# Performance work log

Measured on AMD Instinct MI355X. Metric: run time of the kernel, lower is better.

Reference implementation:

```python
import jax, jax.numpy as jnp
import numpy as np

B_SZ, L, N, H = 8, 4096, 256, 256
R_MIN, R_MAX, MAX_PHASE = 0.0, 1.0, 0.314


def setup_inputs() -> dict:
    key = jax.random.key(0)
    ks = jax.random.split(key, 8)
    x = jax.random.normal(ks[0], (B_SZ, L, H), jnp.float32)
    def glorot(k, shape):
        return jax.random.normal(k, shape, jnp.float32) * jnp.sqrt(2.0 / (shape[0] + shape[1])).astype(jnp.float32)
    B_re = glorot(ks[1], (N, H))
    B_im = glorot(ks[2], (N, H))
    C_re = glorot(ks[3], (H, N))
    C_im = glorot(ks[4], (H, N))
    # DiskRingRadius / DiskRingPhase initializers
    u1 = jax.random.uniform(ks[5], (N,), jnp.float32, 1e-6, 1.0)
    u2 = jax.random.uniform(ks[6], (N,), jnp.float32, 1e-6, 1.0)
    nu_log = jnp.log(-0.5 * jnp.log(u1 * (R_MAX ** 2 - R_MIN ** 2) + R_MIN ** 2))
    theta_log = jnp.log(MAX_PHASE * u2)
    D = jax.random.normal(ks[7], (H,), jnp.float32) * 0.05  # RandomNormal(stddev=0.05)
    return dict(x=x, B_re=B_re, B_im=B_im, C_re=C_re, C_im=C_im,
                nu_log=nu_log, theta_log=theta_log, D=D)


def reference(x, B_re, B_im, C_re, C_im, nu_log, theta_log, D):
    # Diagonal complex recurrence parameters
    Lambda = jnp.exp(jax.lax.complex(-jnp.exp(nu_log), jnp.exp(theta_log)))  # [N]
    gamma = jnp.sqrt(1.0 - jnp.abs(Lambda) ** 2).astype(jnp.complex64)       # [N]
    B_norm = (B_re + 1j * B_im).astype(jnp.complex64) * gamma[:, None]       # [N,H]
    C = (C_re + 1j * C_im).astype(jnp.complex64)                             # [H,N]

    # Input projection: [B,L,N] complex
    Bu = jnp.einsum('blh,nh->bln', x.astype(jnp.complex64), B_norm)
    Lambda_el = jnp.broadcast_to(Lambda, Bu.shape)

    def combine(a, b):
        la, ba = a
        lb, bb = b
        return (la * lb, lb * ba + bb)

    _, states = jax.lax.associative_scan(combine, (Lambda_el, Bu), axis=1)  # [B,L,N]

    y = jnp.real(jnp.einsum('bln,hn->blh', states, C))
    y = y + x * D  # H_in == H -> elementwise skip
    return y
```

## Files before the change

### kernel.cpp

```cpp
#include <hip/hip_runtime.h>
#include <hip/hip_bf16.h>
#include <math.h>

#define B_SZ 8
#define LSEQ 4096
#define NDIM 256
#define HDIM 256
#define MROWS (B_SZ * LSEQ)
#define CH 64
#define NC (LSEQ / CH)

#define BM 64
#define BN 128
#define BK 32
#define PAD 40
#define SSTR 68

typedef _Float16 half8 __attribute__((ext_vector_type(8)));
typedef _Float16 half4 __attribute__((ext_vector_type(4)));
typedef float fx4 __attribute__((ext_vector_type(4)));

__global__ void k_prep(const float* __restrict__ Bre, const float* __restrict__ Bim,
                       const float* __restrict__ Cre, const float* __restrict__ Cim,
                       const float* __restrict__ nu_log, const float* __restrict__ th_log,
                       _Float16* __restrict__ BreH, _Float16* __restrict__ BimH,
                       _Float16* __restrict__ CreH, _Float16* __restrict__ CimNH,
                       float* __restrict__ lamRe, float* __restrict__ lamIm,
                       float* __restrict__ powRe, float* __restrict__ powIm,
                       float* __restrict__ powCRe, float* __restrict__ powCIm) {
    int r = blockIdx.x;
    int t = threadIdx.x;
    float nu  = expf(nu_log[r]);
    float th  = expf(th_log[r]);
    float mod = expf(-nu);
    float g   = sqrtf(fmaxf(1.0f - mod * mod, 0.0f));
    if (t == 0) {
        lamRe[r] = mod * cosf(th);
        lamIm[r] = mod * sinf(th);
    }
    int i = r * 256 + t;
    BreH[i]  = (_Float16)(Bre[i] * g);
    BimH[i]  = (_Float16)(Bim[i] * g);
    CreH[i]  = (_Float16)Cre[i];
    CimNH[i] = (_Float16)(-Cim[i]);
    float nuN = expf(nu_log[t]);
    float thN = expf(th_log[t]);
    if (r < CH) {
        float k  = (float)(r + 1);
        float mo = expf(-nuN * k);
        powRe[r * 256 + t] = mo * cosf(thN * k);
        powIm[r * 256 + t] = mo * sinf(thN * k);
        float kc = (float)(CH * r);
        float mc = expf(-nuN * kc);
        powCRe[r * 256 + t] = mc * cosf(thN * kc);
        powCIm[r * 256 + t] = mc * sinf(thN * kc);
    }
}

__launch_bounds__(256)
__global__ void k_buscan(const float* __restrict__ x,
                         const _Float16* __restrict__ BreH,
                         const _Float16* __restrict__ BimH,
                         const float* __restrict__ lamRe,
                         const float* __restrict__ lamIm,
                         _Float16* __restrict__ stReH,
                         _Float16* __restrict__ stImH,
                         float* __restrict__ finRe,
                         float* __restrict__ finIm) {
    __shared__ __align__(16) _Float16 smem[25600];

    const int tid  = threadIdx.x;
    const int lane = tid & 63;
    const int wave = tid >> 6;
    const int wr   = wave >> 1;
    const int wc   = wave & 1;
    const int m0   = blockIdx.x * BM;
    const int n0   = blockIdx.y * BN;

    const int ar = tid >> 2, ac = (tid & 3) * 8;
    const int br = tid >> 1, bc = (tid & 1) * 16;

    const int fRC = lane & 15;
    const int fKg = (lane >> 4) * 8;

    fx4 accR[8], accI[8];
#pragma unroll
    for (int i = 0; i < 8; ++i) { accR[i] = (fx4)0.0f; accI[i] = (fx4)0.0f; }

    float4 xf0, xf1;
    half8 w0, w1, w2, w3;

    {
        const float* xp = x + (size_t)(m0 + ar) * HDIM + ac;
        xf0 = *(const float4*)xp;
        xf1 = *(const float4*)(xp + 4);
        const _Float16* bp1 = BreH + (size_t)(n0 + br) * HDIM + bc;
        const _Float16* bp2 = BimH + (size_t)(n0 + br) * HDIM + bc;
        w0 = *(const half8*)bp1;  w1 = *(const half8*)(bp1 + 8);
        w2 = *(const half8*)bp2;  w3 = *(const half8*)(bp2 + 8);
        half8 hv;
        hv[0]=(_Float16)xf0.x; hv[1]=(_Float16)xf0.y; hv[2]=(_Float16)xf0.z; hv[3]=(_Float16)xf0.w;
        hv[4]=(_Float16)xf1.x; hv[5]=(_Float16)xf1.y; hv[6]=(_Float16)xf1.z; hv[7]=(_Float16)xf1.w;
        *(half8*)&smem[ar * PAD + ac] = hv;
        *(half8*)&smem[2560 + br * PAD + bc] = w0;  *(half8*)&smem[2560 + br * PAD + bc + 8] = w1;
        *(half8*)&smem[7680 + br * PAD + bc] = w2;  *(half8*)&smem[7680 + br * PAD + bc + 8] = w3;
    }
    __syncthreads();

    int p = 0;
    for (int k0 = 0; k0 < HDIM; k0 += BK) {
        const int po = p * 12800;
        const bool nx = (k0 + BK) < HDIM;
        if (nx) {
            const float* xp = x + (size_t)(m0 + ar) * HDIM + k0 + BK + ac;
            xf0 = *(const float4*)xp;
            xf1 = *(const float4*)(xp + 4);
            const _Float16* bp1 = BreH + (size_t)(n0 + br) * HDIM + k0 + BK + bc;
            const _Float16* bp2 = BimH + (size_t)(n0 + br) * HDIM + k0 + BK + bc;
            w0 = *(const half8*)bp1;  w1 = *(const half8*)(bp1 + 8);
            w2 = *(const half8*)bp2;  w3 = *(const half8*)(bp2 + 8);
        }
        half8 af[2], bRf[4], bIf[4];
#pragma unroll
        for (int sm = 0; sm < 2; ++sm)
            af[sm] = *(const half8*)&smem[po + (wr * 32 + sm * 16 + fRC) * PAD + fKg];
#pragma unroll
        for (int sn = 0; sn < 4; ++sn) {
            bRf[sn] = *(const half8*)&smem[po + 2560 + (wc * 64 + sn * 16 + fRC) * PAD + fKg];
            bIf[sn] = *(const half8*)&smem[po + 7680 + (wc * 64 + sn * 16 + fRC) * PAD + fKg];
        }
#pragma unroll
        for (int sm = 0; sm < 2; ++sm)
#pragma unroll
            for (int sn = 0; sn < 4; ++sn) {
                accR[sm * 4 + sn] = __builtin_amdgcn_mfma_f32_16x16x32_f16(af[sm], bRf[sn], accR[sm * 4 + sn], 0, 0, 0);
                accI[sm * 4 + sn] = __builtin_amdgcn_mfma_f32_16x16x32_f16(af[sm], bIf[sn], accI[sm * 4 + sn], 0, 0, 0);
            }
        if (nx) {
            const int qo = (p ^ 1) * 12800;
            half8 hv;
            hv[0]=(_Float16)xf0.x; hv[1]=(_Float16)xf0.y; hv[2]=(_Float16)xf0.z; hv[3]=(_Float16)xf0.w;
            hv[4]=(_Float16)xf1.x; hv[5]=(_Float16)xf1.y; hv[6]=(_Float16)xf1.z; hv[7]=(_Float16)xf1.w;
            *(half8*)&smem[qo + ar * PAD + ac] = hv;
            *(half8*)&smem[qo + 2560 + br * PAD + bc] = w0;  *(half8*)&smem[qo + 2560 + br * PAD + bc + 8] = w1;
            *(half8*)&smem[qo + 7680 + br * PAD + bc] = w2;  *(half8*)&smem[qo + 7680 + br * PAD + bc + 8] = w3;
        }
        __syncthreads();
        p ^= 1;
    }

    _Float16* SRe = smem;
    _Float16* SIm = smem + 8704;

    const int rBase = (lane >> 4) * 4;
#pragma unroll
    for (int sm = 0; sm < 2; ++sm)
#pragma unroll
        for (int sn = 0; sn < 4; ++sn) {
            int col = wc * 64 + sn * 16 + fRC;
            int row = wr * 32 + sm * 16 + rBase;
            half4 h1, h2;
#pragma unroll
            for (int reg = 0; reg < 4; ++reg) {
                h1[reg] = (_Float16)accR[sm * 4 + sn][reg];
                h2[reg] = (_Float16)accI[sm * 4 + sn][reg];
            }
            *(half4*)&SRe[col * SSTR + row] = h1;
            *(half4*)&SIm[col * SSTR + row] = h2;
        }
    __syncthreads();

    if (tid < BN) {
        int col = tid;
        int n = n0 + col;
        float lr = lamRe[n], li = lamIm[n];
        _Float16* cR = &SRe[col * SSTR];
        _Float16* cI = &SIm[col * SSTR];
        float sr = 0.0f, si = 0.0f;
#pragma unroll 8
        for (int r = 0; r < CH; ++r) {
            float ur = (float)cR[r];
            float ui = (float)cI[r];
            float nr = fmaf(lr, sr, fmaf(-li, si, ur));
            float ni = fmaf(lr, si, fmaf(li, sr, ui));
            sr = nr; si = ni;
            cR[r] = (_Float16)sr;
            cI[r] = (_Float16)si;
        }
        int bb = blockIdx.x >> 6, cc = blockIdx.x & 63;
        size_t f = ((size_t)(bb * NC + cc)) * NDIM + n;
        finRe[f] = sr;
        finIm[f] = si;
    }
    __syncthreads();

    {
        int row = tid >> 2;
        int cb  = (tid & 3) * 32;
        size_t gbase = (size_t)(m0 + row) * NDIM + n0 + cb;
#pragma unroll
        for (int g = 0; g < 4; ++g) {
            half8 h1, h2;
#pragma unroll
            for (int e = 0; e < 8; ++e) {
                int col = cb + g * 8 + e;
                h1[e] = SRe[col * SSTR + row];
                h2[e] = SIm[col * SSTR + row];
            }
            *(half8*)(stReH + gbase + g * 8) = h1;
            *(half8*)(stImH + gbase + g * 8) = h2;
        }
    }
}

__launch_bounds__(256)
__global__ void k_out(const _Float16* __restrict__ sReH,
                      const _Float16* __restrict__ sImH,
                      const _Float16* __restrict__ CreH,
                      const _Float16* __restrict__ CimNH,
                      const float* __restrict__ powRe,
                      const float* __restrict__ powIm,
                      const float* __restrict__ powCRe,
                      const float* __restrict__ powCIm,
                      const float* __restrict__ finRe,
                      const float* __restrict__ finIm,
                      const float* __restrict__ x,
                      const float* __restrict__ Dv,
                      float* __restrict__ y) {
    __shared__ __align__(16) _Float16 A1[2][BM * PAD];
    __shared__ __align__(16) _Float16 A2[2][BM * PAD];
    __shared__ __align__(16) _Float16 Cr[2][BN * PAD];
    __shared__ __align__(16) _Float16 Ci[2][BN * PAD];
    __shared__ __align__(16) float carL[2][NDIM];

    const int tid  = threadIdx.x;
    const int lane = tid & 63;
    const int wave = tid >> 6;
    const int wr   = wave >> 1;
    const int wc   = wave & 1;
    const int m0   = blockIdx.x * BM;
    const int h0   = blockIdx.y * BN;
    const int bb   = blockIdx.x >> 6;
    const int cc   = blockIdx.x & 63;

    const int ar = tid >> 2, ac = (tid & 3) * 8;
    const int br = tid >> 1, bc = (tid & 1) * 16;

    const int fRC = lane & 15;
    const int fKg = (lane >> 4) * 8;

    {
        const int n = tid;
        float cr = 0.0f, ci = 0.0f;
#pragma unroll 4
        for (int j = 0; j < cc; ++j) {
            int k = cc - 1 - j;
            float pr = powCRe[k * NDIM + n];
            float pi = powCIm[k * NDIM + n];
            size_t f = ((size_t)(bb * NC + j)) * NDIM + n;
            float fr = finRe[f];
            float fi = finIm[f];
            cr = fmaf(pr, fr, fmaf(-pi, fi, cr));
            ci = fmaf(pr, fi, fmaf( pi, fr, ci));
        }
        carL[0][n] = cr;
        carL[1][n] = ci;
    }
    __syncthreads();

    fx4 acc[8];
#pragma unroll
    for (int i = 0; i < 8; ++i) acc[i] = (fx4)0.0f;

    half8 s1, s2, c0a, c0b, c1a, c1b;
    float4 pr0, pr1, pi0, pi1, cr0, cr1, ci0, ci1;

#define LOAD_STAGE(K0)                                                          \
    {                                                                           \
        size_t aOff = (size_t)(m0 + ar) * NDIM + (K0) + ac;                     \
        s1 = *(const half8*)(sReH + aOff);                                      \
        s2 = *(const half8*)(sImH + aOff);                                      \
        size_t pOff = (size_t)ar * NDIM + (K0) + ac;                            \
        pr0 = *(const float4*)(powRe + pOff); pr1 = *(const float4*)(powRe + pOff + 4); \
        pi0 = *(const float4*)(powIm + pOff); pi1 = *(const float4*)(powIm + pOff + 4); \
        cr0 = *(const float4*)&carL[0][(K0) + ac]; cr1 = *(const float4*)&carL[0][(K0) + ac + 4]; \
        ci0 = *(const float4*)&carL[1][(K0) + ac]; ci1 = *(const float4*)&carL[1][(K0) + ac + 4]; \
        const _Float16* cp1 = CreH  + (size_t)(h0 + br) * NDIM + (K0) + bc;     \
        const _Float16* cp2 = CimNH + (size_t)(h0 + br) * NDIM + (K0) + bc;     \
        c0a = *(const half8*)cp1;  c0b = *(const half8*)(cp1 + 8);              \
        c1a = *(const half8*)cp2;  c1b = *(const half8*)(cp2 + 8);              \
    }

#define WRITE_STAGE(P)                                                          \
    {                                                                           \
        float prA[8] = {pr0.x,pr0.y,pr0.z,pr0.w,pr1.x,pr1.y,pr1.z,pr1.w};       \
        float piA[8] = {pi0.x,pi0.y,pi0.z,pi0.w,pi1.x,pi1.y,pi1.z,pi1.w};       \
        float crA[8] = {cr0.x,cr0.y,cr0.z,cr0.w,cr1.x,cr1.y,cr1.z,cr1.w};       \
        float ciA[8] = {ci0.x,ci0.y,ci0.z,ci0.w,ci1.x,ci1.y,ci1.z,ci1.w};       \
        half8 h1, h2;                                                           \
        _Pragma("unroll")                                                       \
        for (int e = 0; e < 8; ++e) {                                           \
            float ur = fmaf(prA[e], crA[e], fmaf(-piA[e], ciA[e], (float)s1[e])); \
            float ui = fmaf(prA[e], ciA[e], fmaf( piA[e], crA[e], (float)s2[e])); \
            h1[e] = (_Float16)ur; h2[e] = (_Float16)ui;                         \
        }                                                                       \
        *(half8*)&A1[P][ar * PAD + ac] = h1;                                    \
        *(half8*)&A2[P][ar * PAD + ac] = h2;                                    \
        *(half8*)&Cr[P][br * PAD + bc] = c0a;  *(half8*)&Cr[P][br * PAD + bc + 8] = c0b; \
        *(half8*)&Ci[P][br * PAD + bc] = c1a;  *(half8*)&Ci[P][br * PAD + bc + 8] = c1b; \
    }

    LOAD_STAGE(0);
    WRITE_STAGE(0);
    __syncthreads();

    int p = 0;
    for (int k0 = 0; k0 < NDIM; k0 += BK) {
        const bool nx = (k0 + BK) < NDIM;
        if (nx) LOAD_STAGE(k0 + BK);
        half8 a1[2], a2[2], bRf[4], bIf[4];
#pragma unroll
        for (int sm = 0; sm < 2; ++sm) {
            a1[sm] = *(const half8*)&A1[p][(wr * 32 + sm * 16 + fRC) * PAD + fKg];
            a2[sm] = *(const half8*)&A2[p][(wr * 32 + sm * 16 + fRC) * PAD + fKg];
        }
#pragma unroll
        for (int sn = 0; sn < 4; ++sn) {
            bRf[sn] = *(const half8*)&Cr[p][(wc * 64 + sn * 16 + fRC) * PAD + fKg];
            bIf[sn] = *(const half8*)&Ci[p][(wc * 64 + sn * 16 + fRC) * PAD + fKg];
        }
#pragma unroll
        for (int sm = 0; sm < 2; ++sm)
#pragma unroll
            for (int sn = 0; sn < 4; ++sn) {
                acc[sm * 4 + sn] = __builtin_amdgcn_mfma_f32_16x16x32_f16(a1[sm], bRf[sn], acc[sm * 4 + sn], 0, 0, 0);
                acc[sm * 4 + sn] = __builtin_amdgcn_mfma_f32_16x16x32_f16(a2[sm], bIf[sn], acc[sm * 4 + sn], 0, 0, 0);
            }
        if (nx) WRITE_STAGE(p ^ 1);
        __syncthreads();
        p ^= 1;
    }

    float d[4];
#pragma unroll
    for (int sn = 0; sn < 4; ++sn) d[sn] = Dv[h0 + wc * 64 + sn * 16 + fRC];

    const int rBase = (lane >> 4) * 4;
#pragma unroll
    for (int sm = 0; sm < 2; ++sm)
#pragma unroll
        for (int sn = 0; sn < 4; ++sn) {
            int h = h0 + wc * 64 + sn * 16 + fRC;
#pragma unroll
            for (int reg = 0; reg < 4; ++reg) {
                int m = m0 + wr * 32 + sm * 16 + rBase + reg;
                size_t idx = (size_t)m * HDIM + h;
                y[idx] = fmaf(x[idx], d[sn], acc[sm * 4 + sn][reg]);
            }
        }
#undef LOAD_STAGE
#undef WRITE_STAGE
}

extern "C" void kernel_launch(void* const* d_in, const int* in_sizes, int n_in,
                              void* d_out, int out_size, void* d_ws, size_t ws_size,
                              hipStream_t stream) {
    const float* x      = (const float*)d_in[0];
    const float* B_re   = (const float*)d_in[1];
    const float* B_im   = (const float*)d_in[2];
    const float* C_re   = (const float*)d_in[3];
    const float* C_im   = (const float*)d_in[4];
    const float* nu_log = (const float*)d_in[5];
    const float* th_log = (const float*)d_in[6];
    const float* D      = (const float*)d_in[7];
    float* y = (float*)d_out;

    char* p = (char*)d_ws;
    _Float16* stReH = (_Float16*)p;  p += (size_t)MROWS * NDIM * 2;
    _Float16* stImH = (_Float16*)p;  p += (size_t)MROWS * NDIM * 2;
    _Float16* BreH  = (_Float16*)p;  p += (size_t)NDIM * HDIM * 2;
    _Float16* BimH  = (_Float16*)p;  p += (size_t)NDIM * HDIM * 2;
    _Float16* CreH  = (_Float16*)p;  p += (size_t)HDIM * NDIM * 2;
    _Float16* CimNH = (_Float16*)p;  p += (size_t)HDIM * NDIM * 2;
    float* lamRe  = (float*)p;  p += NDIM * 4;
    float* lamIm  = (float*)p;  p += NDIM * 4;
    float* powRe  = (float*)p;  p += (size_t)CH * NDIM * 4;
    float* powIm  = (float*)p;  p += (size_t)CH * NDIM * 4;
    float* powCRe = (float*)p;  p += (size_t)NC * NDIM * 4;
    float* powCIm = (float*)p;  p += (size_t)NC * NDIM * 4;
    float* finRe  = (float*)p;  p += (size_t)B_SZ * NC * NDIM * 4;
    float* finIm  = (float*)p;  p += (size_t)B_SZ * NC * NDIM * 4;

    k_prep<<<NDIM, 256, 0, stream>>>(B_re, B_im, C_re, C_im, nu_log, th_log,
                                     BreH, BimH, CreH, CimNH, lamRe, lamIm,
                                     powRe, powIm, powCRe, powCIm);

    dim3 gGemm(MROWS / BM, NDIM / BN);
    k_buscan<<<gGemm, 256, 0, stream>>>(x, BreH, BimH, lamRe, lamIm,
                                        stReH, stImH, finRe, finIm);

    dim3 gOut(MROWS / BM, HDIM / BN);
    k_out<<<gOut, 256, 0, stream>>>(stReH, stImH, CreH, CimNH,
                                    powRe, powIm, powCRe, powCIm,
                                    finRe, finIm, x, D, y);
}
```

Before: 164.0 us.

## Load A fragments directly from global and single-buffer weights to cut LDS

In both GEMM kernels the activation (A) operand is now read straight from global memory into MFMA fragment registers instead of going through shared memory. The weight tiles move from double-buffered to single-buffered LDS, with two barriers per k-step. LDS use drops and launch bounds request 4 blocks per CU, aiming at higher occupancy and fewer LDS round trips. The cost is less coalesced global loads for A, more barriers, and no overlap from double buffering.

```diff
diff --git a/kernel.cpp b/kernel.cpp
--- a/kernel.cpp
+++ b/kernel.cpp
@@ -57,7 +57,7 @@
     }
 }
 
-__launch_bounds__(256)
+__launch_bounds__(256, 4)
 __global__ void k_buscan(const float* __restrict__ x,
                          const _Float16* __restrict__ BreH,
                          const _Float16* __restrict__ BimH,
@@ -67,7 +67,7 @@
                          _Float16* __restrict__ stImH,
                          float* __restrict__ finRe,
                          float* __restrict__ finIm) {
-    __shared__ __align__(16) _Float16 smem[25600];
+    __shared__ __align__(16) _Float16 smem[17408];
 
     const int tid  = threadIdx.x;
     const int lane = tid & 63;
@@ -77,57 +77,53 @@
     const int m0   = blockIdx.x * BM;
     const int n0   = blockIdx.y * BN;
 
-    const int ar = tid >> 2, ac = (tid & 3) * 8;
     const int br = tid >> 1, bc = (tid & 1) * 16;
 
     const int fRC = lane & 15;
     const int fKg = (lane >> 4) * 8;
+    const int rowL0 = wr * 32 + fRC;
 
     fx4 accR[8], accI[8];
 #pragma unroll
     for (int i = 0; i < 8; ++i) { accR[i] = (fx4)0.0f; accI[i] = (fx4)0.0f; }
 
-    float4 xf0, xf1;
     half8 w0, w1, w2, w3;
-
     {
-        const float* xp = x + (size_t)(m0 + ar) * HDIM + ac;
-        xf0 = *(const float4*)xp;
-        xf1 = *(const float4*)(xp + 4);
         const _Float16* bp1 = BreH + (size_t)(n0 + br) * HDIM + bc;
         const _Float16* bp2 = BimH + (size_t)(n0 + br) * HDIM + bc;
         w0 = *(const half8*)bp1;  w1 = *(const half8*)(bp1 + 8);
         w2 = *(const half8*)bp2;  w3 = *(const half8*)(bp2 + 8);
-        half8 hv;
-        hv[0]=(_Float16)xf0.x; hv[1]=(_Float16)xf0.y; hv[2]=(_Float16)xf0.z; hv[3]=(_Float16)xf0.w;
-        hv[4]=(_Float16)xf1.x; hv[5]=(_Float16)xf1.y; hv[6]=(_Float16)xf1.z; hv[7]=(_Float16)xf1.w;
-        *(half8*)&smem[ar * PAD + ac] = hv;
-        *(half8*)&smem[2560 + br * PAD + bc] = w0;  *(half8*)&smem[2560 + br * PAD + bc + 8] = w1;
-        *(half8*)&smem[7680 + br * PAD + bc] = w2;  *(half8*)&smem[7680 + br * PAD + bc + 8] = w3;
-    }
-    __syncthreads();
-
-    int p = 0;
+    }
+
     for (int k0 = 0; k0 < HDIM; k0 += BK) {
-        const int po = p * 12800;
+        *(half8*)&smem[br * PAD + bc] = w0;
+        *(half8*)&smem[br * PAD + bc + 8] = w1;
+        *(half8*)&smem[5120 + br * PAD + bc] = w2;
+        *(half8*)&smem[5120 + br * PAD + bc + 8] = w3;
         const bool nx = (k0 + BK) < HDIM;
         if (nx) {
-            const float* xp = x + (size_t)(m0 + ar) * HDIM + k0 + BK + ac;
-            xf0 = *(const float4*)xp;
-            xf1 = *(const float4*)(xp + 4);
             const _Float16* bp1 = BreH + (size_t)(n0 + br) * HDIM + k0 + BK + bc;
             const _Float16* bp2 = BimH + (size_t)(n0 + br) * HDIM + k0 + BK + bc;
             w0 = *(const half8*)bp1;  w1 = *(const half8*)(bp1 + 8);
             w2 = *(const half8*)bp2;  w3 = *(const half8*)(bp2 + 8);
         }
-        half8 af[2], bRf[4], bIf[4];
-#pragma unroll
-        for (int sm = 0; sm < 2; ++sm)
-            af[sm] = *(const half8*)&smem[po + (wr * 32 + sm * 16 + fRC) * PAD + fKg];
+        half8 af[2];
+#pragma unroll
+        for (int sm = 0; sm < 2; ++sm) {
+            const float* xp = x + (size_t)(m0 + rowL0 + sm * 16) * HDIM + k0 + fKg;
+            float4 f0 = *(const float4*)xp;
+            float4 f1 = *(const float4*)(xp + 4);
+            half8 hv;
+            hv[0]=(_Float16)f0.x; hv[1]=(_Float16)f0.y; hv[2]=(_Float16)f0.z; hv[3]=(_Float16)f0.w;
+            hv[4]=(_Float16)f1.x; hv[5]=(_Float16)f1.y; hv[6]=(_Float16)f1.z; hv[7]=(_Float16)f1.w;
+            af[sm] = hv;
+        }
+        __syncthreads();
+        half8 bRf[4], bIf[4];
 #pragma unroll
         for (int sn = 0; sn < 4; ++sn) {
-            bRf[sn] = *(const half8*)&smem[po + 2560 + (wc * 64 + sn * 16 + fRC) * PAD + fKg];
-            bIf[sn] = *(const half8*)&smem[po + 7680 + (wc * 64 + sn * 16 + fRC) * PAD + fKg];
+            bRf[sn] = *(const half8*)&smem[(wc * 64 + sn * 16 + fRC) * PAD + fKg];
+            bIf[sn] = *(const half8*)&smem[5120 + (wc * 64 + sn * 16 + fRC) * PAD + fKg];
         }
 #pragma unroll
         for (int sm = 0; sm < 2; ++sm)
@@ -136,17 +132,7 @@
                 accR[sm * 4 + sn] = __builtin_amdgcn_mfma_f32_16x16x32_f16(af[sm], bRf[sn], accR[sm * 4 + sn], 0, 0, 0);
                 accI[sm * 4 + sn] = __builtin_amdgcn_mfma_f32_16x16x32_f16(af[sm], bIf[sn], accI[sm * 4 + sn], 0, 0, 0);
             }
-        if (nx) {
-            const int qo = (p ^ 1) * 12800;
-            half8 hv;
-            hv[0]=(_Float16)xf0.x; hv[1]=(_Float16)xf0.y; hv[2]=(_Float16)xf0.z; hv[3]=(_Float16)xf0.w;
-            hv[4]=(_Float16)xf1.x; hv[5]=(_Float16)xf1.y; hv[6]=(_Float16)xf1.z; hv[7]=(_Float16)xf1.w;
-            *(half8*)&smem[qo + ar * PAD + ac] = hv;
-            *(half8*)&smem[qo + 2560 + br * PAD + bc] = w0;  *(half8*)&smem[qo + 2560 + br * PAD + bc + 8] = w1;
-            *(half8*)&smem[qo + 7680 + br * PAD + bc] = w2;  *(half8*)&smem[qo + 7680 + br * PAD + bc + 8] = w3;
-        }
         __syncthreads();
-        p ^= 1;
     }
 
     _Float16* SRe = smem;
@@ -213,7 +199,7 @@
     }
 }
 
-__launch_bounds__(256)
+__launch_bounds__(256, 4)
 __global__ void k_out(const _Float16* __restrict__ sReH,
                       const _Float16* __restrict__ sImH,
                       const _Float16* __restrict__ CreH,
@@ -227,10 +213,8 @@
                       const float* __restrict__ x,
                       const float* __restrict__ Dv,
                       float* __restrict__ y) {
-    __shared__ __align__(16) _Float16 A1[2][BM * PAD];
-    __shared__ __align__(16) _Float16 A2[2][BM * PAD];
-    __shared__ __align__(16) _Float16 Cr[2][BN * PAD];
-    __shared__ __align__(16) _Float16 Ci[2][BN * PAD];
+    __shared__ __align__(16) _Float16 Cr[BN * PAD];
+    __shared__ __align__(16) _Float16 Ci[BN * PAD];
     __shared__ __align__(16) float carL[2][NDIM];
 
     const int tid  = threadIdx.x;
@@ -243,11 +227,18 @@
     const int bb   = blockIdx.x >> 6;
     const int cc   = blockIdx.x & 63;
 
-    const int ar = tid >> 2, ac = (tid & 3) * 8;
     const int br = tid >> 1, bc = (tid & 1) * 16;
-
     const int fRC = lane & 15;
     const int fKg = (lane >> 4) * 8;
+    const int rowL0 = wr * 32 + fRC;
+
+    half8 w0, w1, w2, w3;
+    {
+        const _Float16* cp1 = CreH  + (size_t)(h0 + br) * NDIM + bc;
+        const _Float16* cp2 = CimNH + (size_t)(h0 + br) * NDIM + bc;
+        w0 = *(const half8*)cp1;  w1 = *(const half8*)(cp1 + 8);
+        w2 = *(const half8*)cp2;  w3 = *(const half8*)(cp2 + 8);
+    }
 
     {
         const int n = tid;
@@ -272,62 +263,53 @@
 #pragma unroll
     for (int i = 0; i < 8; ++i) acc[i] = (fx4)0.0f;
 
-    half8 s1, s2, c0a, c0b, c1a, c1b;
-    float4 pr0, pr1, pi0, pi1, cr0, cr1, ci0, ci1;
-
-#define LOAD_STAGE(K0)                                                          \
-    {                                                                           \
-        size_t aOff = (size_t)(m0 + ar) * NDIM + (K0) + ac;                     \
-        s1 = *(const half8*)(sReH + aOff);                                      \
-        s2 = *(const half8*)(sImH + aOff);                                      \
-        size_t pOff = (size_t)ar * NDIM + (K0) + ac;                            \
-        pr0 = *(const float4*)(powRe + pOff); pr1 = *(const float4*)(powRe + pOff + 4); \
-        pi0 = *(const float4*)(powIm + pOff); pi1 = *(const float4*)(powIm + pOff + 4); \
-        cr0 = *(const float4*)&carL[0][(K0) + ac]; cr1 = *(const float4*)&carL[0][(K0) + ac + 4]; \
-        ci0 = *(const float4*)&carL[1][(K0) + ac]; ci1 = *(const float4*)&carL[1][(K0) + ac + 4]; \
-        const _Float16* cp1 = CreH  + (size_t)(h0 + br) * NDIM + (K0) + bc;     \
-        const _Float16* cp2 = CimNH + (size_t)(h0 + br) * NDIM + (K0) + bc;     \
-        c0a = *(const half8*)cp1;  c0b = *(const half8*)(cp1 + 8);              \
-        c1a = *(const half8*)cp2;  c1b = *(const half8*)(cp2 + 8);              \
-    }
-
-#define WRITE_STAGE(P)                                                          \
-    {                                                                           \
-        float prA[8] = {pr0.x,pr0.y,pr0.z,pr0.w,pr1.x,pr1.y,pr1.z,pr1.w};       \
-        float piA[8] = {pi0.x,pi0.y,pi0.z,pi0.w,pi1.x,pi1.y,pi1.z,pi1.w};       \
-        float crA[8] = {cr0.x,cr0.y,cr0.z,cr0.w,cr1.x,cr1.y,cr1.z,cr1.w};       \
-        float ciA[8] = {ci0.x,ci0.y,ci0.z,ci0.w,ci1.x,ci1.y,ci1.z,ci1.w};       \
-        half8 h1, h2;                                                           \
-        _Pragma("unroll")                                                       \
-        for (int e = 0; e < 8; ++e) {                                           \
-            float ur = fmaf(prA[e], crA[e], fmaf(-piA[e], ciA[e], (float)s1[e])); \
-            float ui = fmaf(prA[e], ciA[e], fmaf( piA[e], crA[e], (float)s2[e])); \
-            h1[e] = (_Float16)ur; h2[e] = (_Float16)ui;                         \
-        }                                                                       \
-        *(half8*)&A1[P][ar * PAD + ac] = h1;                                    \
-        *(half8*)&A2[P][ar * PAD + ac] = h2;                                    \
-        *(half8*)&Cr[P][br * PAD + bc] = c0a;  *(half8*)&Cr[P][br * PAD + bc + 8] = c0b; \
-        *(half8*)&Ci[P][br * PAD + bc] = c1a;  *(half8*)&Ci[P][br * PAD + bc + 8] = c1b; \
-    }
-
-    LOAD_STAGE(0);
-    WRITE_STAGE(0);
-    __syncthreads();
-
-    int p = 0;
     for (int k0 = 0; k0 < NDIM; k0 += BK) {
+        *(half8*)&Cr[br * PAD + bc] = w0;  *(half8*)&Cr[br * PAD + bc + 8] = w1;
+        *(half8*)&Ci[br * PAD + bc] = w2;  *(half8*)&Ci[br * PAD + bc + 8] = w3;
         const bool nx = (k0 + BK) < NDIM;
-        if (nx) LOAD_STAGE(k0 + BK);
-        half8 a1[2], a2[2], bRf[4], bIf[4];
+        if (nx) {
+            const _Float16* cp1 = CreH  + (size_t)(h0 + br) * NDIM + k0 + BK + bc;
+            const _Float16* cp2 = CimNH + (size_t)(h0 + br) * NDIM + k0 + BK + bc;
+            w0 = *(const half8*)cp1;  w1 = *(const half8*)(cp1 + 8);
+            w2 = *(const half8*)cp2;  w3 = *(const half8*)(cp2 + 8);
+        }
+        half8 a1[2], a2[2];
 #pragma unroll
         for (int sm = 0; sm < 2; ++sm) {
-            a1[sm] = *(const half8*)&A1[p][(wr * 32 + sm * 16 + fRC) * PAD + fKg];
-            a2[sm] = *(const half8*)&A2[p][(wr * 32 + sm * 16 + fRC) * PAD + fKg];
-        }
+            const int rl = rowL0 + sm * 16;
+            size_t aOff = (size_t)(m0 + rl) * NDIM + k0 + fKg;
+            half8 s1 = *(const half8*)(sReH + aOff);
+            half8 s2 = *(const half8*)(sImH + aOff);
+            size_t pOff = (size_t)rl * NDIM + k0 + fKg;
+            float4 pr0 = *(const float4*)(powRe + pOff);
+            float4 pr1 = *(const float4*)(powRe + pOff + 4);
+            float4 pi0 = *(const float4*)(powIm + pOff);
+            float4 pi1 = *(const float4*)(powIm + pOff + 4);
+            float4 c0 = *(const float4*)&carL[0][k0 + fKg];
+            float4 c1 = *(const float4*)&carL[0][k0 + fKg + 4];
+            float4 d0 = *(const float4*)&carL[1][k0 + fKg];
+            float4 d1 = *(const float4*)&carL[1][k0 + fKg + 4];
+            float prA[8] = {pr0.x,pr0.y,pr0.z,pr0.w,pr1.x,pr1.y,pr1.z,pr1.w};
+            float piA[8] = {pi0.x,pi0.y,pi0.z,pi0.w,pi1.x,pi1.y,pi1.z,pi1.w};
+            float crA[8] = {c0.x,c0.y,c0.z,c0.w,c1.x,c1.y,c1.z,c1.w};
+            float ciA[8] = {d0.x,d0.y,d0.z,d0.w,d1.x,d1.y,d1.z,d1.w};
+            half8 h1, h2;
+#pragma unroll
+            for (int e = 0; e < 8; ++e) {
+                float ur = fmaf(prA[e], crA[e], fmaf(-piA[e], ciA[e], (float)s1[e]));
+                float ui = fmaf(prA[e], ciA[e], fmaf( piA[e], crA[e], (float)s2[e]));
+                h1[e] = (_Float16)ur;
+                h2[e] = (_Float16)ui;
+            }
+            a1[sm] = h1;
+            a2[sm] = h2;
+        }
+        __syncthreads();
+        half8 bRf[4], bIf[4];
 #pragma unroll
         for (int sn = 0; sn < 4; ++sn) {
-            bRf[sn] = *(const half8*)&Cr[p][(wc * 64 + sn * 16 + fRC) * PAD + fKg];
-            bIf[sn] = *(const half8*)&Ci[p][(wc * 64 + sn * 16 + fRC) * PAD + fKg];
+            bRf[sn] = *(const half8*)&Cr[(wc * 64 + sn * 16 + fRC) * PAD + fKg];
+            bIf[sn] = *(const half8*)&Ci[(wc * 64 + sn * 16 + fRC) * PAD + fKg];
         }
 #pragma unroll
         for (int sm = 0; sm < 2; ++sm)
@@ -336,9 +318,7 @@
                 acc[sm * 4 + sn] = __builtin_amdgcn_mfma_f32_16x16x32_f16(a1[sm], bRf[sn], acc[sm * 4 + sn], 0, 0, 0);
                 acc[sm * 4 + sn] = __builtin_amdgcn_mfma_f32_16x16x32_f16(a2[sm], bIf[sn], acc[sm * 4 + sn], 0, 0, 0);
             }
-        if (nx) WRITE_STAGE(p ^ 1);
         __syncthreads();
-        p ^= 1;
     }
 
     float d[4];
@@ -358,8 +338,6 @@
                 y[idx] = fmaf(x[idx], d[sn], acc[sm * 4 + sn][reg]);
             }
         }
-#undef LOAD_STAGE
-#undef WRITE_STAGE
 }
 
 extern "C" void kernel_launch(void* const* d_in, const int* in_sizes, int n_in,
```

Result: slower. 215.9 us (+31.7%).
